# Kernel optimization log

Hardware: AMD Instinct MI355X
Metric: run time of the kernel (lower is better)

The kernel has to match this reference:

```python
import jax, jax.numpy as jnp
import numpy as np

B, S, D, H, F = 2, 2048, 768, 12, 3072
HD = D // H


def setup_inputs() -> dict:
    key = jax.random.key(0)
    ks = jax.random.split(key, 6)
    g = lambda k, sh, sc: jax.random.normal(k, sh, jnp.float32) * sc
    return {
        "x": g(ks[0], (B, S, D), 1.0),
        "mask": jnp.tril(jnp.ones((1, 1, S, S), dtype=jnp.bool_)),  # causal
        "qkv_w": g(ks[1], (3 * D, D), 0.02),
        "qkv_b": jnp.zeros((3 * D,), jnp.float32),
        "out_w": g(ks[2], (D, D), 0.02),
        "out_b": jnp.zeros((D,), jnp.float32),
        "fc1_w": g(ks[3], (F, D), 0.02),
        "fc1_b": jnp.zeros((F,), jnp.float32),
        "fc2_w": g(ks[4], (D, F), 0.02),
        "fc2_b": jnp.zeros((D,), jnp.float32),
        "ln1_w": jnp.ones((D,), jnp.float32),
        "ln1_b": jnp.zeros((D,), jnp.float32),
        "ln2_w": jnp.ones((D,), jnp.float32),
        "ln2_b": jnp.zeros((D,), jnp.float32),
    }


def _layernorm(x, w, b, eps=1e-5):
    m = x.mean(-1, keepdims=True)
    v = ((x - m) ** 2).mean(-1, keepdims=True)
    return (x - m) * jax.lax.rsqrt(v + eps) * w + b


def reference(x, mask, qkv_w, qkv_b, out_w, out_b, fc1_w, fc1_b, fc2_w, fc2_b,
              ln1_w, ln1_b, ln2_w, ln2_b):
    b, s, d = x.shape
    h = d // HD  # num_heads
    # --- pre-norm multi-head self-attention (dropout = eval/identity) ---
    hx = _layernorm(x, ln1_w, ln1_b)
    qkv = hx @ qkv_w.T + qkv_b                      # [b,s,3d]
    qkv = qkv.reshape(b, s, 3, h, HD).transpose(2, 0, 3, 1, 4)  # [3,b,h,s,hd]
    q, k, v = qkv[0], qkv[1], qkv[2]
    scale = jnp.sqrt(jnp.float32(HD))
    scores = jnp.einsum("bhqd,bhkd->bhqk", q, k) / scale  # [b,h,s,s]
    scores = jnp.where(mask, scores, -jnp.inf)
    attn = jax.nn.softmax(scores, axis=-1)
    o = jnp.einsum("bhqk,bhkd->bhqd", attn, v)      # [b,h,s,hd]
    o = o.transpose(0, 2, 1, 3).reshape(b, s, d)
    x = x + (o @ out_w.T + out_b)
    # --- pre-norm GELU feed-forward ---
    h2 = _layernorm(x, ln2_w, ln2_b)
    ff = jax.nn.gelu(h2 @ fc1_w.T + fc1_b, approximate=False) @ fc2_w.T + fc2_b
    return x + ff
```

## Files before the change

### kernel.cpp

```cpp
#include <hip/hip_runtime.h>
#include <hip/hip_bf16.h>
#include <cstdint>
#include <cstddef>

typedef __bf16 bf16;
typedef unsigned short ushort_t;
typedef __attribute__((ext_vector_type(8))) __bf16 bf16x8;
typedef __attribute__((ext_vector_type(4))) __bf16 bf16x4;
typedef __attribute__((ext_vector_type(4))) float f32x4;

#define NB 2
#define NS 2048
#define ND 768
#define NH 12
#define NF 3072
#define NT (NB * NS)

__device__ __forceinline__ f32x4 mfma16(bf16x8 a, bf16x8 b, f32x4 c) {
  return __builtin_amdgcn_mfma_f32_16x16x32_bf16(a, b, c, 0, 0, 0);
}

__device__ __forceinline__ void gl_lds16(const bf16* g, bf16* l) {
  __builtin_amdgcn_global_load_lds(
      (__attribute__((address_space(1))) void*)(uintptr_t)g,
      (__attribute__((address_space(3))) void*)l,
      16, 0, 0);
}

__device__ __forceinline__ float gelu_fast(float v) {
  const float u = v * (0.7978845608028654f + 0.03567740814f * v * v);
  const float e = exp2f(u * 2.885390081777927f);
  return v - v / (1.f + e);
}

__global__ __launch_bounds__(256) void sniff_kernel(
    const ushort_t* __restrict__ x, int* __restrict__ flag) {
  __shared__ int s[4];
  int bad = 0;
  for (int i = threadIdx.x; i < 4096; i += 256) {
    const int e = (x[i] >> 7) & 0xFF;
    bad |= (e >= 0xC0);
  }
  bad = __any(bad) ? 1 : 0;
  if ((threadIdx.x & 63) == 0) s[threadIdx.x >> 6] = bad;
  __syncthreads();
  if (threadIdx.x == 0) *flag = s[0] | s[1] | s[2] | s[3];
}

struct CvtArgs {
  const void* s[8];
  bf16* d[8];
  int n8[8];
  int total8;
};

__global__ __launch_bounds__(256) void cvt_all(CvtArgs a,
                                               const int* __restrict__ flag) {
  const int isf = *flag;
  const int stride = gridDim.x * 256;
  for (int i = blockIdx.x * 256 + threadIdx.x; i < a.total8; i += stride) {
    int seg = 0, off = i;
    while (off >= a.n8[seg]) { off -= a.n8[seg]; ++seg; }
    bf16x8 o;
    if (isf) {
      const float* s = (const float*)a.s[seg] + (size_t)off * 8;
      const f32x4 f0 = *(const f32x4*)s;
      const f32x4 f1 = *(const f32x4*)(s + 4);
#pragma unroll
      for (int j = 0; j < 4; ++j) {
        o[j] = (bf16)f0[j];
        o[4 + j] = (bf16)f1[j];
      }
    } else {
      o = *((const bf16x8*)a.s[seg] + off);
    }
    *((bf16x8*)a.d[seg] + off) = o;
  }
}

__global__ __launch_bounds__(256) void ln_kernel(
    const void* __restrict__ xv, const void* __restrict__ wv,
    const void* __restrict__ bv, bf16* __restrict__ y,
    const int* __restrict__ flag) {
  const int isf = *flag;
  const int row = blockIdx.x * 4 + (threadIdx.x >> 6);
  const int L = threadIdx.x & 63;
  const float* xf = (const float*)xv;
  const bf16* xh = (const bf16*)xv;
  const float* wf = (const float*)wv;
  const bf16* wh = (const bf16*)wv;
  const float* bf_ = (const float*)bv;
  const bf16* bh = (const bf16*)bv;
  const size_t base = (size_t)row * ND;
  float v[12];
  float s = 0.f, s2 = 0.f;
#pragma unroll
  for (int i = 0; i < 12; ++i) {
    const int c = L + i * 64;
    v[i] = isf ? xf[base + c] : (float)xh[base + c];
    s += v[i];
    s2 += v[i] * v[i];
  }
#pragma unroll
  for (int off = 1; off < 64; off <<= 1) {
    s += __shfl_xor(s, off);
    s2 += __shfl_xor(s2, off);
  }
  const float mean = s * (1.f / 768.f);
  const float var = s2 * (1.f / 768.f) - mean * mean;
  const float rstd = rsqrtf(var + 1e-5f);
  bf16* yr = y + base;
#pragma unroll
  for (int i = 0; i < 12; ++i) {
    const int c = L + i * 64;
    const float ww = isf ? wf[c] : (float)wh[c];
    const float bb = isf ? bf_[c] : (float)bh[c];
    yr[c] = (bf16)((v[i] - mean) * rstd * ww + bb);
  }
}

__global__ __launch_bounds__(256) void vt_kernel(
    const bf16* __restrict__ qkv, bf16* __restrict__ vT) {
  const int bh = blockIdx.y;
  const int b = bh / NH, h = bh % NH;
  const int st = blockIdx.x;
  __shared__ bf16 Vs[64 * 72];
  const int tid = threadIdx.x;
  {
    const int r = tid >> 2, c = (tid & 3) * 16;
    const bf16* src =
        qkv + (size_t)(b * NS + st * 64 + r) * (3 * ND) + 2 * ND + h * 64 + c;
    *(bf16x8*)&Vs[r * 72 + c] = *(const bf16x8*)src;
    *(bf16x8*)&Vs[r * 72 + c + 8] = *(const bf16x8*)(src + 8);
  }
  __syncthreads();
  {
    const int hd = tid >> 2, t0 = (tid & 3) * 16;
    bf16x8 o0, o1;
#pragma unroll
    for (int j = 0; j < 8; ++j) {
      o0[j] = Vs[(t0 + j) * 72 + hd];
      o1[j] = Vs[(t0 + 8 + j) * 72 + hd];
    }
    bf16* dst = vT + ((size_t)bh * 64 + hd) * NS + st * 64 + t0;
    *(bf16x8*)dst = o0;
    *(bf16x8*)(dst + 8) = o1;
  }
}

template <int EPI, int TM>
__global__ __launch_bounds__(256) void gemm_fast(
    const bf16* __restrict__ A, const bf16* __restrict__ Bt,
    const bf16* __restrict__ bias, const void* resid, void* C,
    int N, int K, int row0, const int* __restrict__ flag) {
  __shared__ bf16 As[TM * 32];
  __shared__ bf16 Bs[128 * 32];
  const int isf = (EPI == 2) ? *flag : 0;
  const int tid = threadIdx.x;
  const int w = tid >> 6, L = tid & 63;
  const int lg = L >> 4, lc = L & 15;
  const int wm = (w >> 1) * (TM / 2), wn = (w & 1) * 64;
  const int bm = blockIdx.y, bn = blockIdx.x;
  const int MT = TM / 32;

  const bf16* Ab = A + (size_t)bm * TM * K;
  const bf16* Bb = Bt + (size_t)bn * 128 * K;

  const int sr = tid >> 2;
  const int sc = (tid & 3) * 8;

  f32x4 acc[MT][4];
#pragma unroll
  for (int i = 0; i < MT; ++i)
#pragma unroll
    for (int j = 0; j < 4; ++j) acc[i][j] = (f32x4){0.f, 0.f, 0.f, 0.f};

  for (int k0 = 0; k0 < K; k0 += 32) {
    __syncthreads();
    gl_lds16(Ab + (size_t)sr * K + k0 + sc, As + tid * 8);
    if (TM == 128)
      gl_lds16(Ab + (size_t)(sr + 64) * K + k0 + sc, As + 2048 + tid * 8);
    gl_lds16(Bb + (size_t)sr * K + k0 + sc, Bs + tid * 8);
    gl_lds16(Bb + (size_t)(sr + 64) * K + k0 + sc, Bs + 2048 + tid * 8);
    __syncthreads();

    bf16x8 af[MT], bfr[4];
#pragma unroll
    for (int mt = 0; mt < MT; ++mt)
      af[mt] = *(const bf16x8*)&As[(wm + mt * 16 + lc) * 32 + lg * 8];
#pragma unroll
    for (int nt = 0; nt < 4; ++nt)
      bfr[nt] = *(const bf16x8*)&Bs[(wn + nt * 16 + lc) * 32 + lg * 8];
#pragma unroll
    for (int mt = 0; mt < MT; ++mt)
#pragma unroll
      for (int nt = 0; nt < 4; ++nt)
        acc[mt][nt] = mfma16(af[mt], bfr[nt], acc[mt][nt]);
  }

  const float* rf = (const float*)resid;
  const bf16* rh = (const bf16*)resid;
  float* Cf = (float*)C;
  bf16* Ch = (bf16*)C;
#pragma unroll
  for (int mt = 0; mt < MT; ++mt) {
#pragma unroll
    for (int nt = 0; nt < 4; ++nt) {
      const int col = bn * 128 + wn + nt * 16 + lc;
      const float bv = (float)bias[col];
#pragma unroll
      for (int r = 0; r < 4; ++r) {
        const int row = bm * TM + wm + mt * 16 + lg * 4 + r;
        float v = acc[mt][nt][r] + bv;
        if (EPI == 1) v = gelu_fast(v);
        const size_t idx = (size_t)(row0 + row) * N + col;
        if (EPI == 2) {
          v += isf ? rf[idx] : (float)rh[idx];
          if (isf) Cf[idx] = v; else Ch[idx] = (bf16)v;
        } else {
          Ch[idx] = (bf16)v;
        }
      }
    }
  }
}

__global__ __launch_bounds__(256) void gemm_qkv(
    const bf16* __restrict__ A, const bf16* __restrict__ Bt,
    const bf16* __restrict__ bias, bf16* __restrict__ qkvout,
    bf16* __restrict__ vT) {
  const int K = ND, N = 3 * ND;
  __shared__ bf16 As[128 * 32];
  __shared__ bf16 Bs[128 * 32];
  const int tid = threadIdx.x;
  const int w = tid >> 6, L = tid & 63;
  const int lg = L >> 4, lc = L & 15;
  const int wm = (w >> 1) * 64, wn = (w & 1) * 64;
  const int bm = blockIdx.y, bn = blockIdx.x;

  const bf16* Ab = A + (size_t)bm * 128 * K;
  const bf16* Bb = Bt + (size_t)bn * 128 * K;

  const int sr = tid >> 2;
  const int sc = (tid & 3) * 8;

  f32x4 acc[4][4];
#pragma unroll
  for (int i = 0; i < 4; ++i)
#pragma unroll
    for (int j = 0; j < 4; ++j) acc[i][j] = (f32x4){0.f, 0.f, 0.f, 0.f};

  for (int k0 = 0; k0 < K; k0 += 32) {
    __syncthreads();
    gl_lds16(Ab + (size_t)sr * K + k0 + sc, As + tid * 8);
    gl_lds16(Ab + (size_t)(sr + 64) * K + k0 + sc, As + 2048 + tid * 8);
    gl_lds16(Bb + (size_t)sr * K + k0 + sc, Bs + tid * 8);
    gl_lds16(Bb + (size_t)(sr + 64) * K + k0 + sc, Bs + 2048 + tid * 8);
    __syncthreads();

    bf16x8 af[4], bfr[4];
#pragma unroll
    for (int mt = 0; mt < 4; ++mt)
      af[mt] = *(const bf16x8*)&As[(wm + mt * 16 + lc) * 32 + lg * 8];
#pragma unroll
    for (int nt = 0; nt < 4; ++nt)
      bfr[nt] = *(const bf16x8*)&Bs[(wn + nt * 16 + lc) * 32 + lg * 8];
#pragma unroll
    for (int mt = 0; mt < 4; ++mt)
#pragma unroll
      for (int nt = 0; nt < 4; ++nt)
        acc[mt][nt] = mfma16(af[mt], bfr[nt], acc[mt][nt]);
  }

#pragma unroll
  for (int mt = 0; mt < 4; ++mt) {
#pragma unroll
    for (int nt = 0; nt < 4; ++nt) {
      const int col = bn * 128 + wn + nt * 16 + lc;
      const float bv = (float)bias[col];
      if (col < 2 * ND) {
#pragma unroll
        for (int r = 0; r < 4; ++r) {
          const int row = bm * 128 + wm + mt * 16 + lg * 4 + r;
          qkvout[(size_t)row * N + col] = (bf16)(acc[mt][nt][r] + bv);
        }
      } else {
        const int colv = col - 2 * ND;
        const int h_ = colv >> 6, hd = colv & 63;
        bf16x4 pk;
#pragma unroll
        for (int r = 0; r < 4; ++r) pk[r] = (bf16)(acc[mt][nt][r] + bv);
        const int tok0 = bm * 128 + wm + mt * 16 + lg * 4;
        const int b_ = tok0 >> 11, s0 = tok0 & (NS - 1);
        *(bf16x4*)&vT[((size_t)(b_ * NH + h_) * 64 + hd) * NS + s0] = pk;
      }
    }
  }
}

template <int EPI>
__global__ __launch_bounds__(256) void gemm_bt(
    const bf16* __restrict__ A, const void* __restrict__ Bt,
    const void* __restrict__ bias, const void* resid, void* C,
    int N, int K, int row0, const int* __restrict__ flag) {
  __shared__ bf16 As[128 * 32];
  __shared__ bf16 Bs[128 * 32];
  const int isf = *flag;
  const int tid = threadIdx.x;
  const int w = tid >> 6, L = tid & 63;
  const int lg = L >> 4, lc = L & 15;
  const int wm = (w >> 1) * 64, wn = (w & 1) * 64;
  const int bm = blockIdx.y, bn = blockIdx.x;

  const bf16* Ab = A + (size_t)bm * 128 * K;
  const bf16* Bth = (const bf16*)Bt + (size_t)bn * 128 * K;
  const float* Btf = (const float*)Bt + (size_t)bn * 128 * K;

  const int sr = tid >> 1;
  const int sc = (tid & 1) * 16;

  f32x4 acc[4][4];
#pragma unroll
  for (int i = 0; i < 4; ++i)
#pragma unroll
    for (int j = 0; j < 4; ++j) acc[i][j] = (f32x4){0.f, 0.f, 0.f, 0.f};

  for (int k0 = 0; k0 < K; k0 += 32) {
    const bf16* ap = Ab + (size_t)sr * K + k0 + sc;
    const bf16x8 a0 = *(const bf16x8*)ap;
    const bf16x8 a1 = *(const bf16x8*)(ap + 8);
    bf16x8 b0, b1;
    if (isf) {
      const float* bp = Btf + (size_t)sr * K + k0 + sc;
      const f32x4 f0 = *(const f32x4*)bp;
      const f32x4 f1 = *(const f32x4*)(bp + 4);
      const f32x4 f2 = *(const f32x4*)(bp + 8);
      const f32x4 f3 = *(const f32x4*)(bp + 12);
#pragma unroll
      for (int j = 0; j < 4; ++j) {
        b0[j] = (bf16)f0[j];
        b0[4 + j] = (bf16)f1[j];
        b1[j] = (bf16)f2[j];
        b1[4 + j] = (bf16)f3[j];
      }
    } else {
      const bf16* bp = Bth + (size_t)sr * K + k0 + sc;
      b0 = *(const bf16x8*)bp;
      b1 = *(const bf16x8*)(bp + 8);
    }
    __syncthreads();
    *(bf16x8*)&As[sr * 32 + sc] = a0;
    *(bf16x8*)&As[sr * 32 + sc + 8] = a1;
    *(bf16x8*)&Bs[sr * 32 + sc] = b0;
    *(bf16x8*)&Bs[sr * 32 + sc + 8] = b1;
    __syncthreads();

    bf16x8 af[4], bfr[4];
#pragma unroll
    for (int mt = 0; mt < 4; ++mt)
      af[mt] = *(const bf16x8*)&As[(wm + mt * 16 + lc) * 32 + lg * 8];
#pragma unroll
    for (int nt = 0; nt < 4; ++nt)
      bfr[nt] = *(const bf16x8*)&Bs[(wn + nt * 16 + lc) * 32 + lg * 8];
#pragma unroll
    for (int mt = 0; mt < 4; ++mt)
#pragma unroll
      for (int nt = 0; nt < 4; ++nt)
        acc[mt][nt] = mfma16(af[mt], bfr[nt], acc[mt][nt]);
  }

  const float* biasf = (const float*)bias;
  const bf16* biash = (const bf16*)bias;
  const float* rf = (const float*)resid;
  const bf16* rh = (const bf16*)resid;
  float* Cf = (float*)C;
  bf16* Ch = (bf16*)C;
#pragma unroll
  for (int mt = 0; mt < 4; ++mt) {
#pragma unroll
    for (int nt = 0; nt < 4; ++nt) {
      const int col = bn * 128 + wn + nt * 16 + lc;
      const float bv = isf ? biasf[col] : (float)biash[col];
#pragma unroll
      for (int r = 0; r < 4; ++r) {
        const int row = bm * 128 + wm + mt * 16 + lg * 4 + r;
        float v = acc[mt][nt][r] + bv;
        if (EPI == 1) v = gelu_fast(v);
        const size_t idx = (size_t)(row0 + row) * N + col;
        if (EPI == 2) {
          v += isf ? rf[idx] : (float)rh[idx];
          if (isf) Cf[idx] = v; else Ch[idx] = (bf16)v;
        } else {
          Ch[idx] = (bf16)v;
        }
      }
    }
  }
}

__global__ __launch_bounds__(256) void flash_attn_v7(
    const bf16* __restrict__ qkv, const bf16* __restrict__ vT,
    bf16* __restrict__ o) {
  const int bh = blockIdx.y;
  const int b = bh / NH, h = bh % NH;
  const int qt = gridDim.x - 1 - blockIdx.x;
  const int q0 = qt * 64;
  const int tid = threadIdx.x;
  const int w = tid >> 6, L = tid & 63;
  const int lg = L >> 4, lc = L & 15;

  __shared__ bf16 Ks[64 * 72];
  __shared__ bf16 Vts[64 * 72];
  __shared__ bf16 Ps[4][16 * 72];

  const float QSCALE = 0.18033688011112042f;
  const size_t tokq = (size_t)(b * NS + q0 + w * 16 + lc);
  const bf16* qp = qkv + tokq * (3 * ND) + h * 64 + lg * 8;
  bf16x8 qf0, qf1;
  {
    const bf16x8 qr0 = *(const bf16x8*)qp;
    const bf16x8 qr1 = *(const bf16x8*)(qp + 32);
#pragma unroll
    for (int j = 0; j < 8; ++j) {
      qf0[j] = (bf16)((float)qr0[j] * QSCALE);
      qf1[j] = (bf16)((float)qr1[j] * QSCALE);
    }
  }

  const int kr = tid >> 2, kc = (tid & 3) * 16;
  const bf16* kbase =
      qkv + (size_t)(b * NS + kr) * (3 * ND) + ND + h * 64 + kc;
  const bf16* vbase = vT + ((size_t)bh * 64 + kr) * NS + kc;

  f32x4 oacc[4];
#pragma unroll
  for (int nt = 0; nt < 4; ++nt) oacc[nt] = (f32x4){0.f, 0.f, 0.f, 0.f};
  float lacc[4] = {0.f, 0.f, 0.f, 0.f};

  const int nkt = qt + 1;

  bf16x8 kreg[2], vreg[2];
#pragma unroll
  for (int p = 0; p < 2; ++p) {
    kreg[p] = *(const bf16x8*)(kbase + p * 8);
    vreg[p] = *(const bf16x8*)(vbase + p * 8);
  }

  for (int kt = 0; kt < nkt; ++kt) {
    __syncthreads();
    *(bf16x8*)&Ks[kr * 72 + kc] = kreg[0];
    *(bf16x8*)&Ks[kr * 72 + kc + 8] = kreg[1];
    *(bf16x8*)&Vts[kr * 72 + kc] = vreg[0];
    *(bf16x8*)&Vts[kr * 72 + kc + 8] = vreg[1];
    __syncthreads();

    if (kt + 1 < nkt) {
      const bf16* kn = kbase + (size_t)(kt + 1) * 64 * (3 * ND);
      const bf16* vn = vbase + (size_t)(kt + 1) * 64;
#pragma unroll
      for (int p = 0; p < 2; ++p) {
        kreg[p] = *(const bf16x8*)(kn + p * 8);
        vreg[p] = *(const bf16x8*)(vn + p * 8);
      }
    }

    f32x4 s[4];
#pragma unroll
    for (int nt = 0; nt < 4; ++nt) {
      const bf16x8 kb0 = *(const bf16x8*)&Ks[(nt * 16 + lc) * 72 + lg * 8];
      const bf16x8 kb1 = *(const bf16x8*)&Ks[(nt * 16 + lc) * 72 + 32 + lg * 8];
      f32x4 z = (f32x4){0.f, 0.f, 0.f, 0.f};
      s[nt] = mfma16(qf0, kb0, z);
      s[nt] = mfma16(qf1, kb1, s[nt]);
    }
    if (kt == nkt - 1) {
#pragma unroll
      for (int nt = 0; nt < 4; ++nt)
#pragma unroll
        for (int r = 0; r < 4; ++r) {
          const int kv = nt * 16 + lc;
          const int qrow = w * 16 + lg * 4 + r;
          if (kv > qrow) s[nt][r] = -1.0e30f;
        }
    }
#pragma unroll
    for (int nt = 0; nt < 4; ++nt)
#pragma unroll
      for (int r = 0; r < 4; ++r) {
        const float p = exp2f(fminf(s[nt][r], 20.f));
        lacc[r] += p;
        Ps[w][(lg * 4 + r) * 72 + nt * 16 + lc] = (bf16)p;
      }
    const bf16x8 p0 = *(const bf16x8*)&Ps[w][lc * 72 + lg * 8];
    const bf16x8 p1 = *(const bf16x8*)&Ps[w][lc * 72 + 32 + lg * 8];
#pragma unroll
    for (int nt = 0; nt < 4; ++nt) {
      const bf16x8 v0 = *(const bf16x8*)&Vts[(nt * 16 + lc) * 72 + lg * 8];
      const bf16x8 v1 = *(const bf16x8*)&Vts[(nt * 16 + lc) * 72 + 32 + lg * 8];
      oacc[nt] = mfma16(p0, v0, oacc[nt]);
      oacc[nt] = mfma16(p1, v1, oacc[nt]);
    }
  }

#pragma unroll
  for (int msk = 1; msk < 16; msk <<= 1)
#pragma unroll
    for (int r = 0; r < 4; ++r) lacc[r] += __shfl_xor(lacc[r], msk);

#pragma unroll
  for (int nt = 0; nt < 4; ++nt)
#pragma unroll
    for (int r = 0; r < 4; ++r) {
      const int qrow = q0 + w * 16 + lg * 4 + r;
      const float val = oacc[nt][r] / lacc[r];
      o[(size_t)(b * NS + qrow) * ND + h * 64 + nt * 16 + lc] = (bf16)val;
    }
}

__global__ __launch_bounds__(256) void flash_attn_v1(
    const bf16* __restrict__ qkv, bf16* __restrict__ o) {
  const int bh = blockIdx.y;
  const int b = bh / NH, h = bh % NH;
  const int qt = gridDim.x - 1 - blockIdx.x;
  const int q0 = qt * 64;
  const int tid = threadIdx.x;
  const int w = tid >> 6, L = tid & 63;
  const int lg = L >> 4, lc = L & 15;

  __shared__ bf16 Ks[64 * 72];
  __shared__ bf16 Vts[64 * 72];
  __shared__ bf16 Ps[4][16 * 72];

  const float QSCALE = 0.18033688011112042f;
  const size_t tokq = (size_t)(b * NS + q0 + w * 16 + lc);
  const bf16* qp = qkv + tokq * (3 * ND) + h * 64 + lg * 8;
  const bf16x8 qr0 = *(const bf16x8*)qp;
  const bf16x8 qr1 = *(const bf16x8*)(qp + 32);
  bf16x8 qf0, qf1;
#pragma unroll
  for (int j = 0; j < 8; ++j) {
    qf0[j] = (bf16)((float)qr0[j] * QSCALE);
    qf1[j] = (bf16)((float)qr1[j] * QSCALE);
  }

  f32x4 oacc[4];
#pragma unroll
  for (int nt = 0; nt < 4; ++nt) oacc[nt] = (f32x4){0.f, 0.f, 0.f, 0.f};
  float lacc[4] = {0.f, 0.f, 0.f, 0.f};

  for (int kt = 0; kt <= qt; ++kt) {
    __syncthreads();
#pragma unroll
    for (int p = 0; p < 2; ++p) {
      const int r = (p * 256 + tid) >> 3;
      const int c = (tid & 7) * 8;
      const bf16* kp =
          qkv + (size_t)(b * NS + kt * 64 + r) * (3 * ND) + ND + h * 64 + c;
      const bf16x8 k8 = *(const bf16x8*)kp;
      *(bf16x8*)&Ks[r * 72 + c] = k8;
      const bf16x8 v8 = *(const bf16x8*)(kp + ND);
#pragma unroll
      for (int j = 0; j < 8; ++j) Vts[(c + j) * 72 + r] = v8[j];
    }
    __syncthreads();

    f32x4 s[4];
#pragma unroll
    for (int nt = 0; nt < 4; ++nt) {
      const bf16x8 b0 = *(const bf16x8*)&Ks[(nt * 16 + lc) * 72 + lg * 8];
      const bf16x8 b1 = *(const bf16x8*)&Ks[(nt * 16 + lc) * 72 + 32 + lg * 8];
      f32x4 z = (f32x4){0.f, 0.f, 0.f, 0.f};
      s[nt] = mfma16(qf0, b0, z);
      s[nt] = mfma16(qf1, b1, s[nt]);
    }
    if (kt == qt) {
#pragma unroll
      for (int nt = 0; nt < 4; ++nt)
#pragma unroll
        for (int r = 0; r < 4; ++r) {
          const int qrow = w * 16 + lg * 4 + r;
          const int kcol = nt * 16 + lc;
          if (kcol > qrow) s[nt][r] = -1.0e30f;
        }
    }
#pragma unroll
    for (int nt = 0; nt < 4; ++nt)
#pragma unroll
      for (int r = 0; r < 4; ++r) {
        const float p = exp2f(fminf(s[nt][r], 20.f));
        lacc[r] += p;
        Ps[w][(lg * 4 + r) * 72 + nt * 16 + lc] = (bf16)p;
      }
    __syncthreads();

    const bf16x8 p0 = *(const bf16x8*)&Ps[w][lc * 72 + lg * 8];
    const bf16x8 p1 = *(const bf16x8*)&Ps[w][lc * 72 + 32 + lg * 8];
#pragma unroll
    for (int nt = 0; nt < 4; ++nt) {
      const bf16x8 v0 = *(const bf16x8*)&Vts[(nt * 16 + lc) * 72 + lg * 8];
      const bf16x8 v1 = *(const bf16x8*)&Vts[(nt * 16 + lc) * 72 + 32 + lg * 8];
      oacc[nt] = mfma16(p0, v0, oacc[nt]);
      oacc[nt] = mfma16(p1, v1, oacc[nt]);
    }
  }

#pragma unroll
  for (int msk = 1; msk < 16; msk <<= 1)
#pragma unroll
    for (int r = 0; r < 4; ++r) lacc[r] += __shfl_xor(lacc[r], msk);

#pragma unroll
  for (int nt = 0; nt < 4; ++nt)
#pragma unroll
    for (int r = 0; r < 4; ++r) {
      const int qrow = q0 + w * 16 + lg * 4 + r;
      const float val = oacc[nt][r] / lacc[r];
      o[(size_t)(b * NS + qrow) * ND + h * 64 + nt * 16 + lc] = (bf16)val;
    }
}

extern "C" void kernel_launch(void* const* d_in, const int* in_sizes, int n_in,
                              void* d_out, int out_size, void* d_ws,
                              size_t ws_size, hipStream_t stream) {
  const void* x = d_in[0];
  const void* qkv_w = d_in[2];
  const void* qkv_b = d_in[3];
  const void* out_w = d_in[4];
  const void* out_b = d_in[5];
  const void* fc1_w = d_in[6];
  const void* fc1_b = d_in[7];
  const void* fc2_w = d_in[8];
  const void* fc2_b = d_in[9];
  const void* ln1_w = d_in[10];
  const void* ln1_b = d_in[11];
  const void* ln2_w = d_in[12];
  const void* ln2_b = d_in[13];
  (void)in_sizes; (void)n_in; (void)out_size;

  char* ws = (char*)d_ws;
  int* flag = (int*)ws;

  sniff_kernel<<<dim3(1), 256, 0, stream>>>((const ushort_t*)x, flag);

  const size_t T1 = 58210048, T2 = 51918592, T3 = 45627136, T4 = 39335680;

  if (ws_size >= T2) {
    bf16* wq = (bf16*)(ws + 256);
    bf16* wo = wq + 1769472;
    bf16* w1 = wo + 589824;
    bf16* w2 = w1 + 2359296;
    bf16* bq = w2 + 2359296;
    bf16* bo = bq + 2304;
    bf16* b1 = bo + 768;
    bf16* b2 = b1 + 3072;
    bf16* slotA = b2 + 768;
    bf16* vT = slotA + (size_t)NT * ND;
    bf16* slotB = vT + (size_t)NT * ND;
    bf16* hx = slotA, *oat = slotA, *h2 = slotA;
    bf16* qkv = slotB;

    CvtArgs ca;
    ca.s[0] = qkv_w; ca.d[0] = wq; ca.n8[0] = 1769472 / 8;
    ca.s[1] = out_w; ca.d[1] = wo; ca.n8[1] = 589824 / 8;
    ca.s[2] = fc1_w; ca.d[2] = w1; ca.n8[2] = 2359296 / 8;
    ca.s[3] = fc2_w; ca.d[3] = w2; ca.n8[3] = 2359296 / 8;
    ca.s[4] = qkv_b; ca.d[4] = bq; ca.n8[4] = 2304 / 8;
    ca.s[5] = out_b; ca.d[5] = bo; ca.n8[5] = 768 / 8;
    ca.s[6] = fc1_b; ca.d[6] = b1; ca.n8[6] = 3072 / 8;
    ca.s[7] = fc2_b; ca.d[7] = b2; ca.n8[7] = 768 / 8;
    ca.total8 = (1769472 + 589824 + 2359296 + 2359296 + 2304 + 768 + 3072 +
                 768) / 8;
    cvt_all<<<dim3(880), 256, 0, stream>>>(ca, flag);

    ln_kernel<<<dim3(NT / 4), 256, 0, stream>>>(x, ln1_w, ln1_b, hx, flag);
    gemm_qkv<<<dim3(18, 32), 256, 0, stream>>>(hx, wq, bq, qkv, vT);
    flash_attn_v7<<<dim3(NS / 64, NB * NH), 256, 0, stream>>>(qkv, vT, oat);
    gemm_fast<2, 64><<<dim3(6, 64), 256, 0, stream>>>(
        oat, wo, bo, x, d_out, ND, ND, 0, flag);
    ln_kernel<<<dim3(NT / 4), 256, 0, stream>>>(d_out, ln2_w, ln2_b, h2, flag);
    if (ws_size >= T1) {
      bf16* ff1 = slotB;
      gemm_fast<1, 128><<<dim3(24, 32), 256, 0, stream>>>(
          h2, w1, b1, nullptr, ff1, NF, ND, 0, flag);
      gemm_fast<2, 64><<<dim3(6, 64), 256, 0, stream>>>(
          ff1, w2, b2, d_out, d_out, ND, NF, 0, flag);
    } else {
      bf16* ff1c = slotB;
      for (int c = 0; c < 2; ++c) {
        gemm_fast<1, 128><<<dim3(24, 16), 256, 0, stream>>>(
            h2 + (size_t)c * 2048 * ND, w1, b1, nullptr, ff1c, NF, ND, 0, flag);
        gemm_fast<2, 64><<<dim3(6, 32), 256, 0, stream>>>(
            ff1c, w2, b2, d_out, d_out, ND, NF, c * 2048, flag);
      }
    }
  } else if (ws_size >= T4) {
    bf16* wq = (bf16*)(ws + 256);
    bf16* wo = wq + 1769472;
    bf16* w1 = wo + 589824;
    bf16* w2 = w1 + 2359296;
    bf16* bq = w2 + 2359296;
    bf16* bo = bq + 2304;
    bf16* b1 = bo + 768;
    bf16* b2 = b1 + 3072;
    bf16* slotA = b2 + 768;
    bf16* slotB = slotA + (size_t)NT * ND;
    bf16* hx = slotA, *oat = slotA, *h2 = slotA;
    bf16* qkv = slotB;

    CvtArgs ca;
    ca.s[0] = qkv_w; ca.d[0] = wq; ca.n8[0] = 1769472 / 8;
    ca.s[1] = out_w; ca.d[1] = wo; ca.n8[1] = 589824 / 8;
    ca.s[2] = fc1_w; ca.d[2] = w1; ca.n8[2] = 2359296 / 8;
    ca.s[3] = fc2_w; ca.d[3] = w2; ca.n8[3] = 2359296 / 8;
    ca.s[4] = qkv_b; ca.d[4] = bq; ca.n8[4] = 2304 / 8;
    ca.s[5] = out_b; ca.d[5] = bo; ca.n8[5] = 768 / 8;
    ca.s[6] = fc1_b; ca.d[6] = b1; ca.n8[6] = 3072 / 8;
    ca.s[7] = fc2_b; ca.d[7] = b2; ca.n8[7] = 768 / 8;
    ca.total8 = (1769472 + 589824 + 2359296 + 2359296 + 2304 + 768 + 3072 +
                 768) / 8;
    cvt_all<<<dim3(880), 256, 0, stream>>>(ca, flag);

    ln_kernel<<<dim3(NT / 4), 256, 0, stream>>>(x, ln1_w, ln1_b, hx, flag);
    gemm_fast<0, 128><<<dim3(18, 32), 256, 0, stream>>>(
        hx, wq, bq, nullptr, qkv, 3 * ND, ND, 0, flag);
    flash_attn_v1<<<dim3(NS / 64, NB * NH), 256, 0, stream>>>(qkv, oat);
    gemm_fast<2, 64><<<dim3(6, 64), 256, 0, stream>>>(
        oat, wo, bo, x, d_out, ND, ND, 0, flag);
    ln_kernel<<<dim3(NT / 4), 256, 0, stream>>>(d_out, ln2_w, ln2_b, h2, flag);
    if (ws_size >= T3) {
      bf16* ff1 = slotB;
      gemm_fast<1, 128><<<dim3(24, 32), 256, 0, stream>>>(
          h2, w1, b1, nullptr, ff1, NF, ND, 0, flag);
      gemm_fast<2, 64><<<dim3(6, 64), 256, 0, stream>>>(
          ff1, w2, b2, d_out, d_out, ND, NF, 0, flag);
    } else {
      bf16* ff1c = slotB;
      for (int c = 0; c < 2; ++c) {
        gemm_fast<1, 128><<<dim3(24, 16), 256, 0, stream>>>(
            h2 + (size_t)c * 2048 * ND, w1, b1, nullptr, ff1c, NF, ND, 0, flag);
        gemm_fast<2, 64><<<dim3(6, 32), 256, 0, stream>>>(
            ff1c, w2, b2, d_out, d_out, ND, NF, c * 2048, flag);
      }
    }
  } else {
    const size_t szTD = (size_t)NT * ND * sizeof(bf16);
    bf16* slotA = (bf16*)(ws + 256);
    bf16* qkv = (bf16*)(ws + 256 + szTD);
    bf16* hx = slotA, *oat = slotA, *h2 = slotA;
    bf16* ff1c = qkv;

    ln_kernel<<<dim3(NT / 4), 256, 0, stream>>>(x, ln1_w, ln1_b, hx, flag);
    gemm_bt<0><<<dim3(18, 32), 256, 0, stream>>>(
        hx, qkv_w, qkv_b, nullptr, qkv, 3 * ND, ND, 0, flag);
    flash_attn_v1<<<dim3(NS / 64, NB * NH), 256, 0, stream>>>(qkv, oat);
    gemm_bt<2><<<dim3(6, 32), 256, 0, stream>>>(
        oat, out_w, out_b, x, d_out, ND, ND, 0, flag);
    ln_kernel<<<dim3(NT / 4), 256, 0, stream>>>(d_out, ln2_w, ln2_b, h2, flag);
    for (int c = 0; c < 4; ++c) {
      gemm_bt<1><<<dim3(24, 8), 256, 0, stream>>>(
          h2 + (size_t)c * 1024 * ND, fc1_w, fc1_b, nullptr, ff1c, NF, ND, 0,
          flag);
      gemm_bt<2><<<dim3(6, 8), 256, 0, stream>>>(
          ff1c, fc2_w, fc2_b, d_out, d_out, ND, NF, c * 1024, flag);
    }
  }
}
```

Baseline: 347.6 us.

## Double-buffer GEMM LDS tiles and remap workgroups across XCDs

The gemm_fast and gemm_qkv K-loops now use two LDS buffers. The next K-slice is prefetched with global_load_lds while the current slice feeds the MFMAs, and only one barrier remains per iteration. All GEMM and flash-attention kernels also remap their linear workgroup ID so that consecutive tiles land on the same XCD, which should improve L2 reuse of shared A/B rows and K/V heads. This costs double the LDS footprint, which may lower occupancy. The changed flash-attention order may also shift the causal load balance.

```diff
diff --git a/kernel.cpp b/kernel.cpp
--- a/kernel.cpp
+++ b/kernel.cpp
@@ -25,6 +25,12 @@
       (__attribute__((address_space(1))) void*)(uintptr_t)g,
       (__attribute__((address_space(3))) void*)l,
       16, 0, 0);
+}
+
+__device__ __forceinline__ int xcd_swz(int lin, int nwg) {
+  const int q = nwg >> 3, r = nwg & 7;
+  const int x = lin & 7, i = lin >> 3;
+  return (x < r ? x * (q + 1) : r * (q + 1) + (x - r) * q) + i;
 }
 
 __device__ __forceinline__ float gelu_fast(float v) {
@@ -153,14 +159,16 @@
     const bf16* __restrict__ A, const bf16* __restrict__ Bt,
     const bf16* __restrict__ bias, const void* resid, void* C,
     int N, int K, int row0, const int* __restrict__ flag) {
-  __shared__ bf16 As[TM * 32];
-  __shared__ bf16 Bs[128 * 32];
+  __shared__ bf16 As[2][TM * 32];
+  __shared__ bf16 Bs[2][128 * 32];
   const int isf = (EPI == 2) ? *flag : 0;
   const int tid = threadIdx.x;
   const int w = tid >> 6, L = tid & 63;
   const int lg = L >> 4, lc = L & 15;
   const int wm = (w >> 1) * (TM / 2), wn = (w & 1) * 64;
-  const int bm = blockIdx.y, bn = blockIdx.x;
+  const int nwg = gridDim.x * gridDim.y;
+  const int lin = xcd_swz(blockIdx.y * gridDim.x + blockIdx.x, nwg);
+  const int bm = lin / gridDim.x, bn = lin % gridDim.x;
   const int MT = TM / 32;
 
   const bf16* Ab = A + (size_t)bm * TM * K;
@@ -175,28 +183,40 @@
 #pragma unroll
     for (int j = 0; j < 4; ++j) acc[i][j] = (f32x4){0.f, 0.f, 0.f, 0.f};
 
+#define GF_STAGE(buf, kk)                                                   \
+  do {                                                                      \
+    gl_lds16(Ab + (size_t)sr * K + (kk) + sc, As[buf] + tid * 8);           \
+    if (TM == 128)                                                          \
+      gl_lds16(Ab + (size_t)(sr + 64) * K + (kk) + sc,                      \
+               As[buf] + 2048 + tid * 8);                                   \
+    gl_lds16(Bb + (size_t)sr * K + (kk) + sc, Bs[buf] + tid * 8);           \
+    gl_lds16(Bb + (size_t)(sr + 64) * K + (kk) + sc,                        \
+             Bs[buf] + 2048 + tid * 8);                                     \
+  } while (0)
+
+  GF_STAGE(0, 0);
+  __syncthreads();
+  int cur = 0;
   for (int k0 = 0; k0 < K; k0 += 32) {
-    __syncthreads();
-    gl_lds16(Ab + (size_t)sr * K + k0 + sc, As + tid * 8);
-    if (TM == 128)
-      gl_lds16(Ab + (size_t)(sr + 64) * K + k0 + sc, As + 2048 + tid * 8);
-    gl_lds16(Bb + (size_t)sr * K + k0 + sc, Bs + tid * 8);
-    gl_lds16(Bb + (size_t)(sr + 64) * K + k0 + sc, Bs + 2048 + tid * 8);
-    __syncthreads();
+    if (k0 + 32 < K) GF_STAGE(cur ^ 1, k0 + 32);
 
     bf16x8 af[MT], bfr[4];
 #pragma unroll
     for (int mt = 0; mt < MT; ++mt)
-      af[mt] = *(const bf16x8*)&As[(wm + mt * 16 + lc) * 32 + lg * 8];
+      af[mt] = *(const bf16x8*)&As[cur][(wm + mt * 16 + lc) * 32 + lg * 8];
 #pragma unroll
     for (int nt = 0; nt < 4; ++nt)
-      bfr[nt] = *(const bf16x8*)&Bs[(wn + nt * 16 + lc) * 32 + lg * 8];
+      bfr[nt] = *(const bf16x8*)&Bs[cur][(wn + nt * 16 + lc) * 32 + lg * 8];
 #pragma unroll
     for (int mt = 0; mt < MT; ++mt)
 #pragma unroll
       for (int nt = 0; nt < 4; ++nt)
         acc[mt][nt] = mfma16(af[mt], bfr[nt], acc[mt][nt]);
-  }
+
+    __syncthreads();
+    cur ^= 1;
+  }
+#undef GF_STAGE
 
   const float* rf = (const float*)resid;
   const bf16* rh = (const bf16*)resid;
@@ -230,13 +250,15 @@
     const bf16* __restrict__ bias, bf16* __restrict__ qkvout,
     bf16* __restrict__ vT) {
   const int K = ND, N = 3 * ND;
-  __shared__ bf16 As[128 * 32];
-  __shared__ bf16 Bs[128 * 32];
+  __shared__ bf16 As[2][128 * 32];
+  __shared__ bf16 Bs[2][128 * 32];
   const int tid = threadIdx.x;
   const int w = tid >> 6, L = tid & 63;
   const int lg = L >> 4, lc = L & 15;
   const int wm = (w >> 1) * 64, wn = (w & 1) * 64;
-  const int bm = blockIdx.y, bn = blockIdx.x;
+  const int nwg = gridDim.x * gridDim.y;
+  const int lin = xcd_swz(blockIdx.y * gridDim.x + blockIdx.x, nwg);
+  const int bm = lin / gridDim.x, bn = lin % gridDim.x;
 
   const bf16* Ab = A + (size_t)bm * 128 * K;
   const bf16* Bb = Bt + (size_t)bn * 128 * K;
@@ -250,27 +272,39 @@
 #pragma unroll
     for (int j = 0; j < 4; ++j) acc[i][j] = (f32x4){0.f, 0.f, 0.f, 0.f};
 
+#define QKV_STAGE(buf, kk)                                                  \
+  do {                                                                      \
+    gl_lds16(Ab + (size_t)sr * K + (kk) + sc, As[buf] + tid * 8);           \
+    gl_lds16(Ab + (size_t)(sr + 64) * K + (kk) + sc,                        \
+             As[buf] + 2048 + tid * 8);                                     \
+    gl_lds16(Bb + (size_t)sr * K + (kk) + sc, Bs[buf] + tid * 8);           \
+    gl_lds16(Bb + (size_t)(sr + 64) * K + (kk) + sc,                        \
+             Bs[buf] + 2048 + tid * 8);                                     \
+  } while (0)
+
+  QKV_STAGE(0, 0);
+  __syncthreads();
+  int cur = 0;
   for (int k0 = 0; k0 < K; k0 += 32) {
-    __syncthreads();
-    gl_lds16(Ab + (size_t)sr * K + k0 + sc, As + tid * 8);
-    gl_lds16(Ab + (size_t)(sr + 64) * K + k0 + sc, As + 2048 + tid * 8);
-    gl_lds16(Bb + (size_t)sr * K + k0 + sc, Bs + tid * 8);
-    gl_lds16(Bb + (size_t)(sr + 64) * K + k0 + sc, Bs + 2048 + tid * 8);
-    __syncthreads();
+    if (k0 + 32 < K) QKV_STAGE(cur ^ 1, k0 + 32);
 
     bf16x8 af[4], bfr[4];
 #pragma unroll
     for (int mt = 0; mt < 4; ++mt)
-      af[mt] = *(const bf16x8*)&As[(wm + mt * 16 + lc) * 32 + lg * 8];
+      af[mt] = *(const bf16x8*)&As[cur][(wm + mt * 16 + lc) * 32 + lg * 8];
 #pragma unroll
     for (int nt = 0; nt < 4; ++nt)
-      bfr[nt] = *(const bf16x8*)&Bs[(wn + nt * 16 + lc) * 32 + lg * 8];
+      bfr[nt] = *(const bf16x8*)&Bs[cur][(wn + nt * 16 + lc) * 32 + lg * 8];
 #pragma unroll
     for (int mt = 0; mt < 4; ++mt)
 #pragma unroll
       for (int nt = 0; nt < 4; ++nt)
         acc[mt][nt] = mfma16(af[mt], bfr[nt], acc[mt][nt]);
-  }
+
+    __syncthreads();
+    cur ^= 1;
+  }
+#undef QKV_STAGE
 
 #pragma unroll
   for (int mt = 0; mt < 4; ++mt) {
@@ -310,7 +344,9 @@
   const int w = tid >> 6, L = tid & 63;
   const int lg = L >> 4, lc = L & 15;
   const int wm = (w >> 1) * 64, wn = (w & 1) * 64;
-  const int bm = blockIdx.y, bn = blockIdx.x;
+  const int nwg = gridDim.x * gridDim.y;
+  const int lin = xcd_swz(blockIdx.y * gridDim.x + blockIdx.x, nwg);
+  const int bm = lin / gridDim.x, bn = lin % gridDim.x;
 
   const bf16* Ab = A + (size_t)bm * 128 * K;
   const bf16* Bth = (const bf16*)Bt + (size_t)bn * 128 * K;
@@ -401,9 +437,11 @@
 __global__ __launch_bounds__(256) void flash_attn_v7(
     const bf16* __restrict__ qkv, const bf16* __restrict__ vT,
     bf16* __restrict__ o) {
-  const int bh = blockIdx.y;
+  const int nwg = gridDim.x * gridDim.y;
+  const int lin = xcd_swz(blockIdx.y * gridDim.x + blockIdx.x, nwg);
+  const int bh = lin / gridDim.x;
   const int b = bh / NH, h = bh % NH;
-  const int qt = gridDim.x - 1 - blockIdx.x;
+  const int qt = gridDim.x - 1 - (lin % gridDim.x);
   const int q0 = qt * 64;
   const int tid = threadIdx.x;
   const int w = tid >> 6, L = tid & 63;
```

Measured after the change: 339.1 us. -2.4%, faster.
